# Kernel optimization log

Hardware: AMD Instinct MI355X
Metric: run time of the kernel (lower is better)

The kernel has to match this reference:

```python
import jax, jax.numpy as jnp
import numpy as np

KS = 3
STRIDE = 2
ALPHA = 16


def _parabolic_kernel(t, ks=KS, alpha=ALPHA):
    # z_i = linspace(-ks//2 + 1, ks//2, ks)  (python floor-div semantics)
    lo = (-ks) // 2 + 1
    hi = ks // 2
    z_i = jnp.linspace(float(lo), float(hi), ks, dtype=jnp.float32)
    z_c = z_i[:, None] ** 2 + z_i[None, :] ** 2            # [ks, ks]
    # per-channel structuring function h: [C, ks, ks]
    return -(z_c[None, :, :] / t[:, None, None]) ** alpha


def setup_inputs() -> dict:
    key = jax.random.key(0)
    kf, kt = jax.random.split(key)
    B, C, H, W = 16, 128, 224, 224
    f = jax.random.normal(kf, (B, C, H, W), dtype=jnp.float32)
    # init='uniform' -> U(0, 4); keep away from 0 to avoid fp32 overflow of (z/t)^16
    t = 0.5 + 3.5 * jax.random.uniform(kt, (C,), dtype=jnp.float32)
    return {"f": f, "t": t}


def reference(f, t):
    # Morphological dilation-style pooling: out = max over window of (f + h)
    h = _parabolic_kernel(t)                               # [C, ks, ks]
    B, C, H, W = f.shape
    Ho = (H - KS) // STRIDE + 1
    Wo = (W - KS) // STRIDE + 1
    out = jnp.full((B, C, Ho, Wo), -jnp.inf, dtype=f.dtype)
    for ki in range(KS):            # fixed 3x3 kernel: small static loop
        for kj in range(KS):
            win = f[:, :, ki:ki + (Ho - 1) * STRIDE + 1:STRIDE,
                          kj:kj + (Wo - 1) * STRIDE + 1:STRIDE]  # [B,C,Ho,Wo]
            out = jnp.maximum(out, win + h[None, :, ki, kj, None, None])
    return out
```

## Files before the change

### kernel.cpp

```cpp
#include <hip/hip_runtime.h>
#include <math.h>


namespace {
constexpr int Bn = 16, Cn = 128, Hn = 224, Wn = 224;
constexpr int KS = 3, STRIDE = 2;
constexpr int Ho = (Hn - KS) / STRIDE + 1;
constexpr int Wo = (Wn - KS) / STRIDE + 1;
}

__global__ __launch_bounds__(256) void lfp_kernel(const float* __restrict__ f,
                                                  const float* __restrict__ t,
                                                  float* __restrict__ out) {
    const int j  = threadIdx.x;
    const int i  = blockIdx.y * 2 + threadIdx.y;
    const int bc = blockIdx.z;
    const int c  = bc & (Cn - 1);

    const float tc = t[c];
    const float xe = 1.0f / tc;
    const float xc = 2.0f / tc;
    float e2 = xe * xe, e4 = e2 * e2, e8 = e4 * e4;
    float c2 = xc * xc, c4 = c2 * c2, c8 = c4 * c4;
    const float h_edge   = -(e8 * e8);
    const float h_corner = -(c8 * c8);

    if (i >= Ho || j >= Wo) return;

    const float* base = f + ((size_t)bc * Hn + (size_t)(2 * i)) * Wn + 2 * j;

    float m = -INFINITY;
#pragma unroll
    for (int ki = 0; ki < 3; ++ki) {
        const float2 v = *(const float2*)(base + (size_t)ki * Wn);
        const float  w = base[(size_t)ki * Wn + 2];
        const float hA = (ki == 1) ? h_edge : h_corner;
        const float hB = (ki == 1) ? 0.0f   : h_edge;
        float rm = fmaxf(fmaxf(v.x + hA, v.y + hB), w + hA);
        m = fmaxf(m, rm);
    }
    out[((size_t)bc * Ho + i) * Wo + j] = m;
}

extern "C" void kernel_launch(void* const* d_in, const int* in_sizes, int n_in,
                              void* d_out, int out_size, void* d_ws, size_t ws_size,
                              hipStream_t stream) {
    const float* f = (const float*)d_in[0];
    const float* t = (const float*)d_in[1];
    float* out = (float*)d_out;

    dim3 block(128, 2, 1);
    dim3 grid(1, (Ho + 1) / 2, Bn * Cn);
    lfp_kernel<<<grid, block, 0, stream>>>(f, t, out);
}
```

Baseline: 545.5 us.

## Compute two outputs per thread with float4 loads and multiple rows per block

Each thread now handles two adjacent output columns using a float4 load plus one extra scalar per input row, which halves the number of load instructions and shares the overlapping middle column. Blocks are reshaped to 64x4 threads, and each thread loops over two output rows, so every block covers eight rows. This cuts the grid size and per-thread setup, including the repeated per-channel kernel computation. In exchange, 8 of the 64 lanes in x sit idle, and the two output stores per thread are strided, so writes coalesce less well.

```diff
diff --git a/kernel.cpp b/kernel.cpp
--- a/kernel.cpp
+++ b/kernel.cpp
@@ -4,42 +4,51 @@
 
 namespace {
 constexpr int Bn = 16, Cn = 128, Hn = 224, Wn = 224;
-constexpr int KS = 3, STRIDE = 2;
-constexpr int Ho = (Hn - KS) / STRIDE + 1;
-constexpr int Wo = (Wn - KS) / STRIDE + 1;
+constexpr int Ho = 111, Wo = 111;
+constexpr int ROWS_PER_BLOCK = 8;
 }
 
 __global__ __launch_bounds__(256) void lfp_kernel(const float* __restrict__ f,
                                                   const float* __restrict__ t,
                                                   float* __restrict__ out) {
     const int j  = threadIdx.x;
-    const int i  = blockIdx.y * 2 + threadIdx.y;
     const int bc = blockIdx.z;
     const int c  = bc & (Cn - 1);
 
     const float tc = t[c];
-    const float xe = 1.0f / tc;
-    const float xc = 2.0f / tc;
+    const float xe = 1.0f / tc, xc = 2.0f / tc;
     float e2 = xe * xe, e4 = e2 * e2, e8 = e4 * e4;
     float c2 = xc * xc, c4 = c2 * c2, c8 = c4 * c4;
-    const float h_edge   = -(e8 * e8);
-    const float h_corner = -(c8 * c8);
+    const float hE = -(e8 * e8);
+    const float hC = -(c8 * c8);
 
-    if (i >= Ho || j >= Wo) return;
+    if (j >= 56) return;
+    const int col  = 4 * j;
+    const int ecol = (col + 4 < Wn) ? col + 4 : Wn - 1;
 
-    const float* base = f + ((size_t)bc * Hn + (size_t)(2 * i)) * Wn + 2 * j;
+    const float* fplane = f + (size_t)bc * Hn * Wn;
+    float* oplane = out + (size_t)bc * Ho * Wo;
 
-    float m = -INFINITY;
 #pragma unroll
-    for (int ki = 0; ki < 3; ++ki) {
-        const float2 v = *(const float2*)(base + (size_t)ki * Wn);
-        const float  w = base[(size_t)ki * Wn + 2];
-        const float hA = (ki == 1) ? h_edge : h_corner;
-        const float hB = (ki == 1) ? 0.0f   : h_edge;
-        float rm = fmaxf(fmaxf(v.x + hA, v.y + hB), w + hA);
-        m = fmaxf(m, rm);
+    for (int ii = 0; ii < 2; ++ii) {
+        const int i = blockIdx.y * ROWS_PER_BLOCK + ii * 4 + threadIdx.y;
+        if (i < Ho) {
+            const float* base = fplane + (size_t)(2 * i) * Wn;
+            float me = -INFINITY, mo = -INFINITY;
+#pragma unroll
+            for (int ki = 0; ki < 3; ++ki) {
+                const float4 v = *(const float4*)(base + (size_t)ki * Wn + col);
+                const float  e = base[(size_t)ki * Wn + ecol];
+                const float hA = (ki == 1) ? hE : hC;
+                const float hB = (ki == 1) ? 0.0f : hE;
+                me = fmaxf(me, fmaxf(fmaxf(v.x + hA, v.y + hB), v.z + hA));
+                mo = fmaxf(mo, fmaxf(fmaxf(v.z + hA, v.w + hB), e + hA));
+            }
+            float* orow = oplane + (size_t)i * Wo;
+            orow[2 * j] = me;
+            if (2 * j + 1 < Wo) orow[2 * j + 1] = mo;
+        }
     }
-    out[((size_t)bc * Ho + i) * Wo + j] = m;
 }
 
 extern "C" void kernel_launch(void* const* d_in, const int* in_sizes, int n_in,
@@ -49,7 +58,7 @@
     const float* t = (const float*)d_in[1];
     float* out = (float*)d_out;
 
-    dim3 block(128, 2, 1);
-    dim3 grid(1, (Ho + 1) / 2, Bn * Cn);
+    dim3 block(64, 4, 1);
+    dim3 grid(1, (Ho + ROWS_PER_BLOCK - 1) / ROWS_PER_BLOCK, Bn * Cn);
     lfp_kernel<<<grid, block, 0, stream>>>(f, t, out);
 }
```

Measured after the change: 560.1 us. 1.03x slower.
